# Kernel tuning notes

Hardware: AMD Instinct MI355X
Metric: run time of the kernel (lower is better)

Reference implementation:

```python
import jax, jax.numpy as jnp
import numpy as np

BN_EPS = 1e-5


def adder2d(x, w, stride=1, padding=1):
    """AdderNet layer: out[b,o,h,w] = -sum_{c,kh,kw} |patch - w|.
    x: [B,C,H,W], w: [O,C,K,K] -> [B,O,Ho,Wo]."""
    B, C, H, W = x.shape
    O, _, K, _ = w.shape
    # patches: [B, C*K*K, Ho, Wo] (feature order = (C, Kh, Kw), matching w.reshape)
    patches = jax.lax.conv_general_dilated_patches(
        x, (K, K), (stride, stride), [(padding, padding), (padding, padding)])
    Bp, F, Ho, Wo = patches.shape
    Xm = patches.transpose(0, 2, 3, 1).reshape(-1, F)  # [N, F], N = B*Ho*Wo
    Wm = w.reshape(O, F)
    # loop over output channels (O small) to avoid a [N, O, F] intermediate
    out = jax.lax.map(lambda wo: -jnp.sum(jnp.abs(Xm - wo), axis=-1), Wm)  # [O, N]
    return out.reshape(O, B, Ho, Wo).transpose(1, 0, 2, 3)


def batchnorm2d(x, gamma, beta):
    # training-mode BN: batch statistics over (B, H, W)
    mean = jnp.mean(x, axis=(0, 2, 3), keepdims=True)
    var = jnp.var(x, axis=(0, 2, 3), keepdims=True)
    inv = jax.lax.rsqrt(var + BN_EPS)
    return (x - mean) * inv * gamma[None, :, None, None] + beta[None, :, None, None]


def setup_inputs() -> dict:
    key = jax.random.key(0)
    ks = jax.random.split(key, 5)
    x = jax.random.normal(ks[0], (256, 1, 64, 64), dtype=jnp.float32)
    w1 = jax.random.normal(ks[1], (16, 1, 3, 3), dtype=jnp.float32) * 0.3
    w2 = jax.random.normal(ks[2], (32, 16, 3, 3), dtype=jnp.float32) * 0.1
    g1 = jnp.ones((16,), jnp.float32); b1 = jnp.zeros((16,), jnp.float32)
    g2 = jnp.ones((32,), jnp.float32); b2 = jnp.zeros((32,), jnp.float32)
    fc_w = jax.random.normal(ks[3], (10, 32), dtype=jnp.float32) * 0.1
    fc_b = jnp.zeros((10,), jnp.float32)
    return {"x": x, "w1": w1, "g1": g1, "b1": b1, "w2": w2,
            "g2": g2, "b2": b2, "fc_w": fc_w, "fc_b": fc_b}


def reference(x, w1, g1, b1, w2, g2, b2, fc_w, fc_b):
    h = jax.nn.relu(batchnorm2d(adder2d(x, w1), g1, b1))   # [B,16,64,64]
    h = jax.nn.relu(batchnorm2d(adder2d(h, w2), g2, b2))   # [B,32,64,64]
    h = jnp.mean(h, axis=(2, 3))                            # adaptive avg pool -> [B,32]
    return h @ fc_w.T + fc_b                                # [B,10]
```

## Files before the change

### kernel.cpp

```cpp
#include <hip/hip_runtime.h>
#include <hip/hip_fp16.h>


#define BATCH 256
#define HW 4096

typedef unsigned int u32;
typedef unsigned long long u64;
typedef __attribute__((ext_vector_type(4))) unsigned int u32x4;

__device__ __forceinline__ u32x4 mqsad(u64 src, u32 ref, u32x4 acc) {
#if __has_builtin(__builtin_amdgcn_mqsad_u32_u8)
  return __builtin_amdgcn_mqsad_u32_u8(src, ref, acc);
#else
  u32x4 d;
  asm("v_mqsad_u32_u8 %0, %1, %2, %3"
      : "=&v"(d)
      : "v"(src), "v"(ref), "v"(acc));
  return d;
#endif
}

__global__ __launch_bounds__(256, 4) void k_stats1(const float* __restrict__ x,
                                                   const float* __restrict__ w1,
                                                   double* __restrict__ s1,
                                                   const float* __restrict__ w2,
                                                   u32* __restrict__ w2b,
                                                   __half* __restrict__ y1) {
  __shared__ float sx[18 * 66];
  __shared__ float red[4 * 16 * 2];
  int blk = blockIdx.x, tid = threadIdx.x;
  int b = blk >> 2, row0 = (blk & 3) * 16;

  if (blk == 0) {
    for (int i = tid; i < 512; i += 256) {
      int oc = i >> 4, c = i & 15;
      int og = oc >> 3, o = oc & 7;
      const float* wp = w2 + (oc * 16 + c) * 9;
      u32 q[9];
#pragma unroll
      for (int t = 0; t < 9; t++) {
        float qf = rintf(fmaf(wp[t], 32.f, 48.f));
        q[t] = (u32)fminf(fmaxf(qf, 1.f), 255.f);
      }
      u32* dst = w2b + ((og * 16 + c) * 8 + o) * 3;
      dst[0] = q[0] | (q[1] << 8) | (q[2] << 16);
      dst[1] = q[3] | (q[4] << 8) | (q[5] << 16);
      dst[2] = q[6] | (q[7] << 8) | (q[8] << 16);
    }
  }

  const float* xb = x + b * HW;
  for (int i = tid; i < 18 * 66; i += 256) {
    int r = i / 66, cc = i - r * 66;
    int ry = row0 + r - 1, rx = cc - 1;
    sx[i] = (ry >= 0 && ry < 64 && rx >= 0 && rx < 64) ? xb[ry * 64 + rx] : 0.f;
  }
  __syncthreads();

  int col = tid & 63, rr4 = tid >> 6;
  float pa[4][9];
#pragma unroll
  for (int k = 0; k < 4; k++) {
    int rloc = rr4 * 4 + k;
#pragma unroll
    for (int dy = 0; dy < 3; dy++)
#pragma unroll
      for (int dx = 0; dx < 3; dx++)
        pa[k][dy * 3 + dx] = sx[(rloc + dy) * 66 + col + dx];
  }
  float tsum[16], tsq[16];
#pragma unroll
  for (int c = 0; c < 16; c++) { tsum[c] = 0.f; tsq[c] = 0.f; }
#pragma unroll
  for (int c = 0; c < 16; c++) {
    float wv[9];
#pragma unroll
    for (int t = 0; t < 9; t++) wv[t] = w1[c * 9 + t];
    __half* yc = y1 + (((size_t)(b * 16 + c)) << 12);
#pragma unroll
    for (int k = 0; k < 4; k++) {
      float acc = 0.f;
#pragma unroll
      for (int t = 0; t < 9; t++) acc += fabsf(pa[k][t] - wv[t]);
      float v = -acc;
      tsum[c] += v;
      tsq[c] = fmaf(v, v, tsq[c]);
      yc[((row0 + rr4 * 4 + k) << 6) + col] = __float2half(v);
    }
  }
  int lane = tid & 63, wid = tid >> 6;
#pragma unroll
  for (int c = 0; c < 16; c++) {
    float s = tsum[c], q = tsq[c];
    for (int off = 32; off; off >>= 1) {
      s += __shfl_down(s, off, 64);
      q += __shfl_down(q, off, 64);
    }
    if (lane == 0) { red[(wid * 16 + c) * 2] = s; red[(wid * 16 + c) * 2 + 1] = q; }
  }
  __syncthreads();
  if (tid < 16) {
    float s = red[tid * 2] + red[(16 + tid) * 2] + red[(32 + tid) * 2] + red[(48 + tid) * 2];
    float q = red[tid * 2 + 1] + red[(16 + tid) * 2 + 1] + red[(32 + tid) * 2 + 1] +
              red[(48 + tid) * 2 + 1];
    atomicAdd(&s1[tid], (double)s);
    atomicAdd(&s1[16 + tid], (double)q);
  }
}

__global__ __launch_bounds__(512, 8) void k_layer2(
    const __half* __restrict__ y1, const double* __restrict__ s1,
    const float* __restrict__ g1, const float* __restrict__ b1,
    const u32* __restrict__ w2b, __half* __restrict__ a2,
    double* __restrict__ s2) {
  __shared__ __align__(16) unsigned char shu[16 * 800];
  __shared__ float red[8 * 8];
  __shared__ float sc1s[16], sf1s[16];
  int blk = blockIdx.x;
  int b = blk >> 3, y0 = (blk & 7) << 3;
  int tid = threadIdx.x;

  if (tid < 16) {
    double N = 1048576.0;
    double mean = s1[tid] / N;
    double var = s1[16 + tid] / N - mean * mean;
    float inv = (float)(1.0 / sqrt(var + 1e-5));
    float sc = g1[tid] * inv;
    float sf = b1[tid] - (float)mean * sc;
    sc1s[tid] = sc * 32.f;
    sf1s[tid] = fmaf(sf, 32.f, 48.5f);
  }
  __syncthreads();

#pragma unroll 1
  for (int p = 0; p < 3; p++) {
    int jj = p * 512 + tid;
    if (jj < 1280) {
      int rowjob = jj >> 3, kq = jj & 7;
      int ch = rowjob / 10;
      int rr = rowjob - ch * 10;
      int gr = y0 + rr - 1;
      float sc8 = sc1s[ch], sf8 = sf1s[ch];
      u32 B[8];
      if (gr >= 0 && gr < 64) {
        uint4 v = *reinterpret_cast<const uint4*>(
            y1 + (((size_t)(b * 16 + ch)) << 12) + (gr << 6) + (kq << 3));
        const u32* vd = reinterpret_cast<const u32*>(&v);
#pragma unroll
        for (int q = 0; q < 4; q++) {
          float2 f = __half22float2(*reinterpret_cast<const __half2*>(&vd[q]));
          float t0 = fmaf(f.x, sc8, sf8);
          float t1 = fmaf(f.y, sc8, sf8);
          B[q * 2] = (u32)fminf(fmaxf(t0, 48.5f), 255.f);
          B[q * 2 + 1] = (u32)fminf(fmaxf(t1, 48.5f), 255.f);
        }
      } else {
#pragma unroll
        for (int q = 0; q < 8; q++) B[q] = 48u;
      }
      u32 prev = (u32)__shfl_up((int)B[7], 1, 64);
      if (kq == 0) prev = 48u;
      u32 d0 = prev | (B[0] << 8) | (B[1] << 16) | (B[2] << 24);
      u32 d1 = B[3] | (B[4] << 8) | (B[5] << 16) | (B[6] << 24);
      unsigned char* dst = shu + rowjob * 80 + (kq << 3);
      *reinterpret_cast<uint2*>(dst) = make_uint2(d0, d1);
      if (kq == 7)
        *reinterpret_cast<u32*>(dst + 8) = B[7] | 0x30303000u;
    }
  }
  __syncthreads();

  int lane = tid & 63;
  int w8 = tid >> 6;
  int og = w8 >> 1, half = w8 & 1;
  int wofs = __builtin_amdgcn_readfirstlane(og * 384 + half * 12);
  const u32* wbase = w2b + wofs;
  int r = lane >> 3;
  int x0 = (lane & 7) << 3;
  const unsigned char* shb = shu + r * 80 + x0;

  u32x4 acc[4][2];
#pragma unroll
  for (int o = 0; o < 4; o++) {
    acc[o][0] = (u32x4)(0u);
    acc[o][1] = (u32x4)(0u);
  }

  u64 Aa[3], Ab[3];
  u32 Ma[3], Mb[3];
  u32 Wa[12], Wb[12];

#define LOADC(Av, Mv, Wv, cc)                                     \
  do {                                                            \
    const unsigned char* rp_ = shb + (cc) * 800;                  \
    _Pragma("unroll") for (int dy_ = 0; dy_ < 3; dy_++) {         \
      Av[dy_] = *reinterpret_cast<const u64*>(rp_ + dy_ * 80);    \
      Mv[dy_] = *reinterpret_cast<const u32*>(rp_ + dy_ * 80 + 8);\
    }                                                             \
    const u32* wc_ = wbase + (cc) * 24;                           \
    _Pragma("unroll") for (int j_ = 0; j_ < 12; j_++) Wv[j_] = wc_[j_]; \
  } while (0)

#define COMPUTE(Av, Mv, Wv)                                       \
  do {                                                            \
    _Pragma("unroll") for (int dy_ = 0; dy_ < 3; dy_++) {         \
      u64 lo_ = Av[dy_];                                          \
      u64 hi_ = (Av[dy_] >> 32) | ((u64)Mv[dy_] << 32);           \
      _Pragma("unroll") for (int o_ = 0; o_ < 4; o_++) {          \
        u32 wr_ = Wv[o_ * 3 + dy_];                               \
        acc[o_][0] = mqsad(lo_, wr_, acc[o_][0]);                 \
        acc[o_][1] = mqsad(hi_, wr_, acc[o_][1]);                 \
      }                                                           \
    }                                                             \
  } while (0)

  LOADC(Aa, Ma, Wa, 0);
#pragma unroll 1
  for (int c = 0; c < 16; c += 2) {
    LOADC(Ab, Mb, Wb, c + 1);
    COMPUTE(Aa, Ma, Wa);
    if (c < 14) LOADC(Aa, Ma, Wa, c + 2);
    COMPUTE(Ab, Mb, Wb);
  }
#undef LOADC
#undef COMPUTE

  const float ksc = -1.f / 32.f;
  __half* a2b = a2 + ((size_t)b * 32 + og * 8 + half * 4) * HW + (y0 + r) * 64 + x0;
#pragma unroll
  for (int o = 0; o < 4; o++) {
    float f0 = (float)acc[o][0].x * ksc, f1 = (float)acc[o][0].y * ksc;
    float f2 = (float)acc[o][0].z * ksc, f3 = (float)acc[o][0].w * ksc;
    float f4 = (float)acc[o][1].x * ksc, f5 = (float)acc[o][1].y * ksc;
    float f6 = (float)acc[o][1].z * ksc, f7 = (float)acc[o][1].w * ksc;
    __half2 h01 = __floats2half2_rn(f0, f1);
    __half2 h23 = __floats2half2_rn(f2, f3);
    __half2 h45 = __floats2half2_rn(f4, f5);
    __half2 h67 = __floats2half2_rn(f6, f7);
    uint4 st = make_uint4(*reinterpret_cast<u32*>(&h01), *reinterpret_cast<u32*>(&h23),
                          *reinterpret_cast<u32*>(&h45), *reinterpret_cast<u32*>(&h67));
    *reinterpret_cast<uint4*>(a2b + o * HW) = st;
    float2 c0 = __half22float2(h01), c1 = __half22float2(h23);
    float2 c2 = __half22float2(h45), c3 = __half22float2(h67);
    float s = c0.x + c0.y + c1.x + c1.y + c2.x + c2.y + c3.x + c3.y;
    float q = c0.x * c0.x + c0.y * c0.y + c1.x * c1.x + c1.y * c1.y +
              c2.x * c2.x + c2.y * c2.y + c3.x * c3.x + c3.y * c3.y;
    for (int off = 32; off; off >>= 1) {
      s += __shfl_down(s, off, 64);
      q += __shfl_down(q, off, 64);
    }
    if (lane == 0) { red[w8 * 8 + o * 2] = s; red[w8 * 8 + o * 2 + 1] = q; }
  }
  __syncthreads();
  if (tid < 32) {
    int oc = tid;
    int ww = (oc >> 3) * 2 + ((oc >> 2) & 1);
    int oo = oc & 3;
    float s = red[ww * 8 + oo * 2];
    float q = red[ww * 8 + oo * 2 + 1];
    atomicAdd(&s2[oc], (double)s);
    atomicAdd(&s2[32 + oc], (double)q);
  }
}

__global__ __launch_bounds__(1024) void k_poolfc(const __half* __restrict__ a2,
                                                 const double* __restrict__ s2,
                                                 const float* __restrict__ g2,
                                                 const float* __restrict__ b2,
                                                 const float* __restrict__ fw,
                                                 const float* __restrict__ fb,
                                                 float* __restrict__ out) {
  __shared__ float sc2s[32], sf2s[32];
  __shared__ float poolv[32];
  int b = blockIdx.x, tid = threadIdx.x;
  if (tid < 32) {
    double N = 1048576.0;
    double mean = s2[tid] / N;
    double var = s2[32 + tid] / N - mean * mean;
    float inv = (float)(1.0 / sqrt(var + 1e-5));
    float sc = g2[tid] * inv;
    sc2s[tid] = sc;
    sf2s[tid] = b2[tid] - (float)mean * sc;
  }
  __syncthreads();
  int o = tid >> 5, part = tid & 31;
  const uint4* p = (const uint4*)(a2 + ((size_t)b * 32 + o) * HW);
  float s = sc2s[o], f = sf2s[o];
  float acc = 0.f;
#pragma unroll
  for (int i = 0; i < 16; i++) {
    uint4 v = p[i * 32 + part];
    float2 f0 = __half22float2(*reinterpret_cast<const __half2*>(&v.x));
    float2 f1 = __half22float2(*reinterpret_cast<const __half2*>(&v.y));
    float2 f2 = __half22float2(*reinterpret_cast<const __half2*>(&v.z));
    float2 f3 = __half22float2(*reinterpret_cast<const __half2*>(&v.w));
    acc += fmaxf(fmaf(f0.x, s, f), 0.f) + fmaxf(fmaf(f0.y, s, f), 0.f) +
           fmaxf(fmaf(f1.x, s, f), 0.f) + fmaxf(fmaf(f1.y, s, f), 0.f) +
           fmaxf(fmaf(f2.x, s, f), 0.f) + fmaxf(fmaf(f2.y, s, f), 0.f) +
           fmaxf(fmaf(f3.x, s, f), 0.f) + fmaxf(fmaf(f3.y, s, f), 0.f);
  }
  acc += __shfl_down(acc, 16, 32);
  acc += __shfl_down(acc, 8, 32);
  acc += __shfl_down(acc, 4, 32);
  acc += __shfl_down(acc, 2, 32);
  acc += __shfl_down(acc, 1, 32);
  if (part == 0) poolv[o] = acc * (1.f / 4096.f);
  __syncthreads();
  if (tid < 10) {
    float rr = fb[tid];
#pragma unroll
    for (int oc = 0; oc < 32; oc++) rr += poolv[oc] * fw[tid * 32 + oc];
    out[b * 10 + tid] = rr;
  }
}

extern "C" void kernel_launch(void* const* d_in, const int* in_sizes, int n_in,
                              void* d_out, int out_size, void* d_ws, size_t ws_size,
                              hipStream_t stream) {
  const float* x   = (const float*)d_in[0];
  const float* w1  = (const float*)d_in[1];
  const float* g1  = (const float*)d_in[2];
  const float* b1  = (const float*)d_in[3];
  const float* w2  = (const float*)d_in[4];
  const float* g2  = (const float*)d_in[5];
  const float* b2  = (const float*)d_in[6];
  const float* fcw = (const float*)d_in[7];
  const float* fcb = (const float*)d_in[8];
  float* out = (float*)d_out;

  char* ws = (char*)d_ws;
  __half* a2 = (__half*)ws;
  double* stats = (double*)(ws + 67108864);
  double* s1 = stats;
  double* s2 = stats + 32;
  u32* w2b = (u32*)(ws + 67108864 + 1024);
  __half* y1 = (__half*)(ws + 67108864 + 16384);

  hipMemsetAsync(stats, 0, 768, stream);
  k_stats1<<<1024, 256, 0, stream>>>(x, w1, s1, w2, w2b, y1);
  k_layer2<<<2048, 512, 0, stream>>>(y1, s1, g1, b1, w2b, a2, s2);
  k_poolfc<<<256, 1024, 0, stream>>>(a2, s2, g2, b2, fcw, fcb, out);
}
```

Before: 197.2 us.

## Fuse three kernels into one persistent kernel with software grid barriers

Merges the layer-1 stats, layer-2 adder, and pool/FC kernels into a single 256-block, 1024-thread kernel (one block per image) separated by atomic-counter grid barriers. The aim is to remove two kernel launch boundaries and their tail idle time, and to cut the per-block atomics for BN statistics. The cost is fewer, larger blocks with serial loops over row tiles, so less parallelism to hide latency. The barrier assumes all 256 blocks are co-resident and includes a spin timeout, so correctness depends on occupancy; the first block's w2 quantisation is also not ordered before other blocks read it until the first barrier.

```diff
diff --git a/kernel.cpp b/kernel.cpp
--- a/kernel.cpp
+++ b/kernel.cpp
@@ -2,7 +2,6 @@
 #include <hip/hip_fp16.h>
 
 
-#define BATCH 256
 #define HW 4096
 
 typedef unsigned int u32;
@@ -21,105 +20,111 @@
 #endif
 }
 
-__global__ __launch_bounds__(256, 4) void k_stats1(const float* __restrict__ x,
-                                                   const float* __restrict__ w1,
-                                                   double* __restrict__ s1,
-                                                   const float* __restrict__ w2,
-                                                   u32* __restrict__ w2b,
-                                                   __half* __restrict__ y1) {
-  __shared__ float sx[18 * 66];
-  __shared__ float red[4 * 16 * 2];
+__device__ __forceinline__ void gbar(u32* ctr, u32 tgt) {
+  __syncthreads();
+  if (threadIdx.x == 0) {
+    __threadfence();
+    __hip_atomic_fetch_add(ctr, 1u, __ATOMIC_ACQ_REL, __HIP_MEMORY_SCOPE_AGENT);
+    u32 n = 0;
+    while (__hip_atomic_load(ctr, __ATOMIC_ACQUIRE, __HIP_MEMORY_SCOPE_AGENT) < tgt &&
+           ++n < (1u << 21)) {
+      __builtin_amdgcn_s_sleep(2);
+    }
+    __threadfence();
+  }
+  __syncthreads();
+}
+
+__global__ __launch_bounds__(1024, 4) void k_fused(
+    const float* __restrict__ x, const float* __restrict__ w1,
+    const float* __restrict__ g1, const float* __restrict__ b1,
+    const float* __restrict__ w2, const float* __restrict__ g2,
+    const float* __restrict__ b2, const float* __restrict__ fw,
+    const float* __restrict__ fb, float* __restrict__ out,
+    double* s1, double* s2, u32* ctr, u32* w2b,
+    __half* __restrict__ y1, __half* __restrict__ a2) {
+  __shared__ __align__(16) unsigned char smem[25600];
+  __shared__ float red[512];
+  __shared__ float p1a[16], p1b[16], p2a[32], p2b[32], poolv[32];
   int blk = blockIdx.x, tid = threadIdx.x;
-  int b = blk >> 2, row0 = (blk & 3) * 16;
-
-  if (blk == 0) {
-    for (int i = tid; i < 512; i += 256) {
-      int oc = i >> 4, c = i & 15;
-      int og = oc >> 3, o = oc & 7;
-      const float* wp = w2 + (oc * 16 + c) * 9;
-      u32 q[9];
-#pragma unroll
-      for (int t = 0; t < 9; t++) {
-        float qf = rintf(fmaf(wp[t], 32.f, 48.f));
-        q[t] = (u32)fminf(fmaxf(qf, 1.f), 255.f);
-      }
-      u32* dst = w2b + ((og * 16 + c) * 8 + o) * 3;
-      dst[0] = q[0] | (q[1] << 8) | (q[2] << 16);
-      dst[1] = q[3] | (q[4] << 8) | (q[5] << 16);
-      dst[2] = q[6] | (q[7] << 8) | (q[8] << 16);
-    }
-  }
-
-  const float* xb = x + b * HW;
-  for (int i = tid; i < 18 * 66; i += 256) {
-    int r = i / 66, cc = i - r * 66;
-    int ry = row0 + r - 1, rx = cc - 1;
-    sx[i] = (ry >= 0 && ry < 64 && rx >= 0 && rx < 64) ? xb[ry * 64 + rx] : 0.f;
-  }
-  __syncthreads();
-
-  int col = tid & 63, rr4 = tid >> 6;
-  float pa[4][9];
-#pragma unroll
-  for (int k = 0; k < 4; k++) {
-    int rloc = rr4 * 4 + k;
-#pragma unroll
-    for (int dy = 0; dy < 3; dy++)
-#pragma unroll
-      for (int dx = 0; dx < 3; dx++)
-        pa[k][dy * 3 + dx] = sx[(rloc + dy) * 66 + col + dx];
-  }
+  int b = blk;
+
+  if (blk == 0 && tid < 512) {
+    int oc = tid >> 4, c = tid & 15;
+    int og = oc >> 3, o = oc & 7;
+    const float* wp = w2 + (oc * 16 + c) * 9;
+    u32 q[9];
+#pragma unroll
+    for (int t = 0; t < 9; t++) {
+      float qf = rintf(fmaf(wp[t], 32.f, 48.f));
+      q[t] = (u32)fminf(fmaxf(qf, 1.f), 255.f);
+    }
+    u32* dst = w2b + ((og * 16 + c) * 8 + o) * 3;
+    dst[0] = q[0] | (q[1] << 8) | (q[2] << 16);
+    dst[1] = q[3] | (q[4] << 8) | (q[5] << 16);
+    dst[2] = q[6] | (q[7] << 8) | (q[8] << 16);
+  }
+
   float tsum[16], tsq[16];
 #pragma unroll
   for (int c = 0; c < 16; c++) { tsum[c] = 0.f; tsq[c] = 0.f; }
-#pragma unroll
-  for (int c = 0; c < 16; c++) {
-    float wv[9];
-#pragma unroll
-    for (int t = 0; t < 9; t++) wv[t] = w1[c * 9 + t];
-    __half* yc = y1 + (((size_t)(b * 16 + c)) << 12);
-#pragma unroll
-    for (int k = 0; k < 4; k++) {
-      float acc = 0.f;
-#pragma unroll
-      for (int t = 0; t < 9; t++) acc += fabsf(pa[k][t] - wv[t]);
-      float v = -acc;
-      tsum[c] += v;
-      tsq[c] = fmaf(v, v, tsq[c]);
-      yc[((row0 + rr4 * 4 + k) << 6) + col] = __float2half(v);
-    }
-  }
-  int lane = tid & 63, wid = tid >> 6;
-#pragma unroll
-  for (int c = 0; c < 16; c++) {
-    float s = tsum[c], q = tsq[c];
-    for (int off = 32; off; off >>= 1) {
-      s += __shfl_down(s, off, 64);
-      q += __shfl_down(q, off, 64);
-    }
-    if (lane == 0) { red[(wid * 16 + c) * 2] = s; red[(wid * 16 + c) * 2 + 1] = q; }
-  }
-  __syncthreads();
-  if (tid < 16) {
-    float s = red[tid * 2] + red[(16 + tid) * 2] + red[(32 + tid) * 2] + red[(48 + tid) * 2];
-    float q = red[tid * 2 + 1] + red[(16 + tid) * 2 + 1] + red[(32 + tid) * 2 + 1] +
-              red[(48 + tid) * 2 + 1];
-    atomicAdd(&s1[tid], (double)s);
-    atomicAdd(&s1[16 + tid], (double)q);
-  }
-}
-
-__global__ __launch_bounds__(512, 8) void k_layer2(
-    const __half* __restrict__ y1, const double* __restrict__ s1,
-    const float* __restrict__ g1, const float* __restrict__ b1,
-    const u32* __restrict__ w2b, __half* __restrict__ a2,
-    double* __restrict__ s2) {
-  __shared__ __align__(16) unsigned char shu[16 * 800];
-  __shared__ float red[8 * 8];
-  __shared__ float sc1s[16], sf1s[16];
-  int blk = blockIdx.x;
-  int b = blk >> 3, y0 = (blk & 7) << 3;
-  int tid = threadIdx.x;
+  {
+    int col = tid & 63, wr = tid >> 6;
+    const float* xb = x + b * HW;
+#pragma unroll 1
+    for (int q4 = 0; q4 < 4; q4++) {
+      int row0 = q4 * 16;
+      float* sx = (float*)smem;
+      __syncthreads();
+      for (int i = tid; i < 18 * 66; i += 1024) {
+        int rr = i / 66, cc = i - rr * 66;
+        int ry = row0 + rr - 1, rx = cc - 1;
+        sx[i] = (ry >= 0 && ry < 64 && rx >= 0 && rx < 64) ? xb[ry * 64 + rx] : 0.f;
+      }
+      __syncthreads();
+      float pa[9];
+#pragma unroll
+      for (int dy = 0; dy < 3; dy++)
+#pragma unroll
+        for (int dx = 0; dx < 3; dx++)
+          pa[dy * 3 + dx] = sx[(wr + dy) * 66 + col + dx];
+#pragma unroll
+      for (int c = 0; c < 16; c++) {
+        float wv[9];
+#pragma unroll
+        for (int t = 0; t < 9; t++) wv[t] = w1[c * 9 + t];
+        float acc = 0.f;
+#pragma unroll
+        for (int t = 0; t < 9; t++) acc += fabsf(pa[t] - wv[t]);
+        float v = -acc;
+        tsum[c] += v;
+        tsq[c] = fmaf(v, v, tsq[c]);
+        y1[(((size_t)(b * 16 + c)) << 12) + ((row0 + wr) << 6) + col] = __float2half(v);
+      }
+    }
+    int lane = tid & 63;
+#pragma unroll
+    for (int c = 0; c < 16; c++) {
+      float s = tsum[c], qv = tsq[c];
+      for (int off = 32; off; off >>= 1) {
+        s += __shfl_down(s, off, 64);
+        qv += __shfl_down(qv, off, 64);
+      }
+      if (lane == 0) { red[(wr * 16 + c) * 2] = s; red[(wr * 16 + c) * 2 + 1] = qv; }
+    }
+    __syncthreads();
+    if (tid < 16) {
+      float s = 0.f, qv = 0.f;
+#pragma unroll
+      for (int w = 0; w < 16; w++) {
+        s += red[(w * 16 + tid) * 2];
+        qv += red[(w * 16 + tid) * 2 + 1];
+      }
+      atomicAdd(&s1[tid], (double)s);
+      atomicAdd(&s1[16 + tid], (double)qv);
+    }
+  }
+  gbar(ctr + 0, 256);
 
   if (tid < 16) {
     double N = 1048576.0;
@@ -128,68 +133,76 @@
     float inv = (float)(1.0 / sqrt(var + 1e-5));
     float sc = g1[tid] * inv;
     float sf = b1[tid] - (float)mean * sc;
-    sc1s[tid] = sc * 32.f;
-    sf1s[tid] = fmaf(sf, 32.f, 48.5f);
-  }
-  __syncthreads();
+    p1a[tid] = sc * 32.f;
+    p1b[tid] = fmaf(sf, 32.f, 48.5f);
+  }
+  __syncthreads();
+
+  {
+    int th = tid & 511, hb = tid >> 9;
+    int lane = tid & 63;
+    int w8 = (tid >> 6) & 7;
+    int og = w8 >> 1, half = w8 & 1;
+    int wofs = __builtin_amdgcn_readfirstlane(og * 384 + half * 12);
+    const u32* wbase = w2b + wofs;
+    int r = lane >> 3, x0 = (lane & 7) << 3;
+    unsigned char* shu = smem + hb * 12800;
+    const unsigned char* shb = shu + r * 80 + x0;
+
+    float ssum[4], ssq[4];
+#pragma unroll
+    for (int o = 0; o < 4; o++) { ssum[o] = 0.f; ssq[o] = 0.f; }
 
 #pragma unroll 1
-  for (int p = 0; p < 3; p++) {
-    int jj = p * 512 + tid;
-    if (jj < 1280) {
-      int rowjob = jj >> 3, kq = jj & 7;
-      int ch = rowjob / 10;
-      int rr = rowjob - ch * 10;
-      int gr = y0 + rr - 1;
-      float sc8 = sc1s[ch], sf8 = sf1s[ch];
-      u32 B[8];
-      if (gr >= 0 && gr < 64) {
-        uint4 v = *reinterpret_cast<const uint4*>(
-            y1 + (((size_t)(b * 16 + ch)) << 12) + (gr << 6) + (kq << 3));
-        const u32* vd = reinterpret_cast<const u32*>(&v);
-#pragma unroll
-        for (int q = 0; q < 4; q++) {
-          float2 f = __half22float2(*reinterpret_cast<const __half2*>(&vd[q]));
-          float t0 = fmaf(f.x, sc8, sf8);
-          float t1 = fmaf(f.y, sc8, sf8);
-          B[q * 2] = (u32)fminf(fmaxf(t0, 48.5f), 255.f);
-          B[q * 2 + 1] = (u32)fminf(fmaxf(t1, 48.5f), 255.f);
+    for (int pr = 0; pr < 4; pr++) {
+      int y0 = (pr * 2 + hb) * 8;
+      __syncthreads();
+
+#pragma unroll 1
+      for (int pp = 0; pp < 3; pp++) {
+        int jj = pp * 512 + th;
+        if (jj < 1280) {
+          int rowjob = jj >> 3, kq = jj & 7;
+          int ch = rowjob / 10;
+          int rr = rowjob - ch * 10;
+          int gr = y0 + rr - 1;
+          float sc8 = p1a[ch], sf8 = p1b[ch];
+          u32 B[8];
+          if (gr >= 0 && gr < 64) {
+            uint4 v = *reinterpret_cast<const uint4*>(
+                y1 + (((size_t)(b * 16 + ch)) << 12) + (gr << 6) + (kq << 3));
+            const u32* vd = reinterpret_cast<const u32*>(&v);
+#pragma unroll
+            for (int qq = 0; qq < 4; qq++) {
+              float2 f = __half22float2(*reinterpret_cast<const __half2*>(&vd[qq]));
+              float t0 = fmaf(f.x, sc8, sf8);
+              float t1 = fmaf(f.y, sc8, sf8);
+              B[qq * 2] = (u32)fminf(fmaxf(t0, 48.5f), 255.f);
+              B[qq * 2 + 1] = (u32)fminf(fmaxf(t1, 48.5f), 255.f);
+            }
+          } else {
+#pragma unroll
+            for (int qq = 0; qq < 8; qq++) B[qq] = 48u;
+          }
+          u32 prev = (u32)__shfl_up((int)B[7], 1, 64);
+          if (kq == 0) prev = 48u;
+          u32 d0 = prev | (B[0] << 8) | (B[1] << 16) | (B[2] << 24);
+          u32 d1 = B[3] | (B[4] << 8) | (B[5] << 16) | (B[6] << 24);
+          unsigned char* dst = shu + rowjob * 80 + (kq << 3);
+          *reinterpret_cast<uint2*>(dst) = make_uint2(d0, d1);
+          if (kq == 7)
+            *reinterpret_cast<u32*>(dst + 8) = B[7] | 0x30303000u;
         }
-      } else {
-#pragma unroll
-        for (int q = 0; q < 8; q++) B[q] = 48u;
-      }
-      u32 prev = (u32)__shfl_up((int)B[7], 1, 64);
-      if (kq == 0) prev = 48u;
-      u32 d0 = prev | (B[0] << 8) | (B[1] << 16) | (B[2] << 24);
-      u32 d1 = B[3] | (B[4] << 8) | (B[5] << 16) | (B[6] << 24);
-      unsigned char* dst = shu + rowjob * 80 + (kq << 3);
-      *reinterpret_cast<uint2*>(dst) = make_uint2(d0, d1);
-      if (kq == 7)
-        *reinterpret_cast<u32*>(dst + 8) = B[7] | 0x30303000u;
-    }
-  }
-  __syncthreads();
-
-  int lane = tid & 63;
-  int w8 = tid >> 6;
-  int og = w8 >> 1, half = w8 & 1;
-  int wofs = __builtin_amdgcn_readfirstlane(og * 384 + half * 12);
-  const u32* wbase = w2b + wofs;
-  int r = lane >> 3;
-  int x0 = (lane & 7) << 3;
-  const unsigned char* shb = shu + r * 80 + x0;
-
-  u32x4 acc[4][2];
-#pragma unroll
-  for (int o = 0; o < 4; o++) {
-    acc[o][0] = (u32x4)(0u);
-    acc[o][1] = (u32x4)(0u);
-  }
-
-  u64 Aa[3], Ab[3];
-  u32 Ma[3], Mb[3];
-  u32 Wa[12], Wb[12];
+      }
+      __syncthreads();
+
+      u32x4 acc[4][2];
+#pragma unroll
+      for (int o = 0; o < 4; o++) { acc[o][0] = (u32x4)(0u); acc[o][1] = (u32x4)(0u); }
+
+      u64 Aa[3], Ab[3];
+      u32 Ma[3], Mb[3];
+      u32 Wa[12], Wb[12];
 
 #define LOADC(Av, Mv, Wv, cc)                                     \
   do {                                                            \
@@ -215,98 +228,102 @@
     }                                                             \
   } while (0)
 
-  LOADC(Aa, Ma, Wa, 0);
+      LOADC(Aa, Ma, Wa, 0);
 #pragma unroll 1
-  for (int c = 0; c < 16; c += 2) {
-    LOADC(Ab, Mb, Wb, c + 1);
-    COMPUTE(Aa, Ma, Wa);
-    if (c < 14) LOADC(Aa, Ma, Wa, c + 2);
-    COMPUTE(Ab, Mb, Wb);
-  }
+      for (int c = 0; c < 16; c += 2) {
+        LOADC(Ab, Mb, Wb, c + 1);
+        COMPUTE(Aa, Ma, Wa);
+        if (c < 14) LOADC(Aa, Ma, Wa, c + 2);
+        COMPUTE(Ab, Mb, Wb);
+      }
 #undef LOADC
 #undef COMPUTE
 
-  const float ksc = -1.f / 32.f;
-  __half* a2b = a2 + ((size_t)b * 32 + og * 8 + half * 4) * HW + (y0 + r) * 64 + x0;
-#pragma unroll
-  for (int o = 0; o < 4; o++) {
-    float f0 = (float)acc[o][0].x * ksc, f1 = (float)acc[o][0].y * ksc;
-    float f2 = (float)acc[o][0].z * ksc, f3 = (float)acc[o][0].w * ksc;
-    float f4 = (float)acc[o][1].x * ksc, f5 = (float)acc[o][1].y * ksc;
-    float f6 = (float)acc[o][1].z * ksc, f7 = (float)acc[o][1].w * ksc;
-    __half2 h01 = __floats2half2_rn(f0, f1);
-    __half2 h23 = __floats2half2_rn(f2, f3);
-    __half2 h45 = __floats2half2_rn(f4, f5);
-    __half2 h67 = __floats2half2_rn(f6, f7);
-    uint4 st = make_uint4(*reinterpret_cast<u32*>(&h01), *reinterpret_cast<u32*>(&h23),
-                          *reinterpret_cast<u32*>(&h45), *reinterpret_cast<u32*>(&h67));
-    *reinterpret_cast<uint4*>(a2b + o * HW) = st;
-    float2 c0 = __half22float2(h01), c1 = __half22float2(h23);
-    float2 c2 = __half22float2(h45), c3 = __half22float2(h67);
-    float s = c0.x + c0.y + c1.x + c1.y + c2.x + c2.y + c3.x + c3.y;
-    float q = c0.x * c0.x + c0.y * c0.y + c1.x * c1.x + c1.y * c1.y +
-              c2.x * c2.x + c2.y * c2.y + c3.x * c3.x + c3.y * c3.y;
-    for (int off = 32; off; off >>= 1) {
-      s += __shfl_down(s, off, 64);
-      q += __shfl_down(q, off, 64);
-    }
-    if (lane == 0) { red[w8 * 8 + o * 2] = s; red[w8 * 8 + o * 2 + 1] = q; }
-  }
-  __syncthreads();
-  if (tid < 32) {
-    int oc = tid;
-    int ww = (oc >> 3) * 2 + ((oc >> 2) & 1);
-    int oo = oc & 3;
-    float s = red[ww * 8 + oo * 2];
-    float q = red[ww * 8 + oo * 2 + 1];
-    atomicAdd(&s2[oc], (double)s);
-    atomicAdd(&s2[32 + oc], (double)q);
-  }
-}
-
-__global__ __launch_bounds__(1024) void k_poolfc(const __half* __restrict__ a2,
-                                                 const double* __restrict__ s2,
-                                                 const float* __restrict__ g2,
-                                                 const float* __restrict__ b2,
-                                                 const float* __restrict__ fw,
-                                                 const float* __restrict__ fb,
-                                                 float* __restrict__ out) {
-  __shared__ float sc2s[32], sf2s[32];
-  __shared__ float poolv[32];
-  int b = blockIdx.x, tid = threadIdx.x;
+      const float ksc = -1.f / 32.f;
+      __half* a2b =
+          a2 + ((size_t)b * 32 + og * 8 + half * 4) * HW + (y0 + r) * 64 + x0;
+#pragma unroll
+      for (int o = 0; o < 4; o++) {
+        float f0 = (float)acc[o][0].x * ksc, f1 = (float)acc[o][0].y * ksc;
+        float f2 = (float)acc[o][0].z * ksc, f3 = (float)acc[o][0].w * ksc;
+        float f4 = (float)acc[o][1].x * ksc, f5 = (float)acc[o][1].y * ksc;
+        float f6 = (float)acc[o][1].z * ksc, f7 = (float)acc[o][1].w * ksc;
+        __half2 h01 = __floats2half2_rn(f0, f1);
+        __half2 h23 = __floats2half2_rn(f2, f3);
+        __half2 h45 = __floats2half2_rn(f4, f5);
+        __half2 h67 = __floats2half2_rn(f6, f7);
+        uint4 st = make_uint4(*reinterpret_cast<u32*>(&h01), *reinterpret_cast<u32*>(&h23),
+                              *reinterpret_cast<u32*>(&h45), *reinterpret_cast<u32*>(&h67));
+        *reinterpret_cast<uint4*>(a2b + o * HW) = st;
+        float2 c0 = __half22float2(h01), c1 = __half22float2(h23);
+        float2 c2 = __half22float2(h45), c3 = __half22float2(h67);
+        ssum[o] += c0.x + c0.y + c1.x + c1.y + c2.x + c2.y + c3.x + c3.y;
+        ssq[o] += c0.x * c0.x + c0.y * c0.y + c1.x * c1.x + c1.y * c1.y +
+                  c2.x * c2.x + c2.y * c2.y + c3.x * c3.x + c3.y * c3.y;
+      }
+    }
+
+#pragma unroll
+    for (int o = 0; o < 4; o++) {
+      float s = ssum[o], qv = ssq[o];
+      for (int off = 32; off; off >>= 1) {
+        s += __shfl_down(s, off, 64);
+        qv += __shfl_down(qv, off, 64);
+      }
+      if (lane == 0) {
+        red[(hb * 8 + w8) * 8 + o * 2] = s;
+        red[(hb * 8 + w8) * 8 + o * 2 + 1] = qv;
+      }
+    }
+    __syncthreads();
+    if (tid < 32) {
+      int oc = tid;
+      int ww = (oc >> 3) * 2 + ((oc >> 2) & 1);
+      int oo = oc & 3;
+      float s = red[ww * 8 + oo * 2] + red[(8 + ww) * 8 + oo * 2];
+      float qv = red[ww * 8 + oo * 2 + 1] + red[(8 + ww) * 8 + oo * 2 + 1];
+      atomicAdd(&s2[oc], (double)s);
+      atomicAdd(&s2[32 + oc], (double)qv);
+    }
+  }
+  gbar(ctr + 1, 256);
+
   if (tid < 32) {
     double N = 1048576.0;
     double mean = s2[tid] / N;
     double var = s2[32 + tid] / N - mean * mean;
     float inv = (float)(1.0 / sqrt(var + 1e-5));
     float sc = g2[tid] * inv;
-    sc2s[tid] = sc;
-    sf2s[tid] = b2[tid] - (float)mean * sc;
-  }
-  __syncthreads();
-  int o = tid >> 5, part = tid & 31;
-  const uint4* p = (const uint4*)(a2 + ((size_t)b * 32 + o) * HW);
-  float s = sc2s[o], f = sf2s[o];
-  float acc = 0.f;
-#pragma unroll
-  for (int i = 0; i < 16; i++) {
-    uint4 v = p[i * 32 + part];
-    float2 f0 = __half22float2(*reinterpret_cast<const __half2*>(&v.x));
-    float2 f1 = __half22float2(*reinterpret_cast<const __half2*>(&v.y));
-    float2 f2 = __half22float2(*reinterpret_cast<const __half2*>(&v.z));
-    float2 f3 = __half22float2(*reinterpret_cast<const __half2*>(&v.w));
-    acc += fmaxf(fmaf(f0.x, s, f), 0.f) + fmaxf(fmaf(f0.y, s, f), 0.f) +
-           fmaxf(fmaf(f1.x, s, f), 0.f) + fmaxf(fmaf(f1.y, s, f), 0.f) +
-           fmaxf(fmaf(f2.x, s, f), 0.f) + fmaxf(fmaf(f2.y, s, f), 0.f) +
-           fmaxf(fmaf(f3.x, s, f), 0.f) + fmaxf(fmaf(f3.y, s, f), 0.f);
-  }
-  acc += __shfl_down(acc, 16, 32);
-  acc += __shfl_down(acc, 8, 32);
-  acc += __shfl_down(acc, 4, 32);
-  acc += __shfl_down(acc, 2, 32);
-  acc += __shfl_down(acc, 1, 32);
-  if (part == 0) poolv[o] = acc * (1.f / 4096.f);
-  __syncthreads();
+    p2a[tid] = sc;
+    p2b[tid] = b2[tid] - (float)mean * sc;
+  }
+  __syncthreads();
+  {
+    int oc = tid >> 5, part = tid & 31;
+    const uint4* p = (const uint4*)(a2 + ((size_t)b * 32 + oc) * HW);
+    float s = p2a[oc], f = p2b[oc];
+    float acc = 0.f;
+#pragma unroll
+    for (int i = 0; i < 16; i++) {
+      uint4 v = p[i * 32 + part];
+      float2 f0 = __half22float2(*reinterpret_cast<const __half2*>(&v.x));
+      float2 f1 = __half22float2(*reinterpret_cast<const __half2*>(&v.y));
+      float2 f2 = __half22float2(*reinterpret_cast<const __half2*>(&v.z));
+      float2 f3 = __half22float2(*reinterpret_cast<const __half2*>(&v.w));
+      acc += fmaxf(fmaf(f0.x, s, f), 0.f) + fmaxf(fmaf(f0.y, s, f), 0.f) +
+             fmaxf(fmaf(f1.x, s, f), 0.f) + fmaxf(fmaf(f1.y, s, f), 0.f) +
+             fmaxf(fmaf(f2.x, s, f), 0.f) + fmaxf(fmaf(f2.y, s, f), 0.f) +
+             fmaxf(fmaf(f3.x, s, f), 0.f) + fmaxf(fmaf(f3.y, s, f), 0.f);
+    }
+    acc += __shfl_down(acc, 16, 32);
+    acc += __shfl_down(acc, 8, 32);
+    acc += __shfl_down(acc, 4, 32);
+    acc += __shfl_down(acc, 2, 32);
+    acc += __shfl_down(acc, 1, 32);
+    if (part == 0) poolv[oc] = acc * (1.f / 4096.f);
+  }
+  __syncthreads();
+
   if (tid < 10) {
     float rr = fb[tid];
 #pragma unroll
@@ -334,11 +351,11 @@
   double* stats = (double*)(ws + 67108864);
   double* s1 = stats;
   double* s2 = stats + 32;
+  u32* ctr = (u32*)(ws + 67108864 + 768);
   u32* w2b = (u32*)(ws + 67108864 + 1024);
   __half* y1 = (__half*)(ws + 67108864 + 16384);
 
-  hipMemsetAsync(stats, 0, 768, stream);
-  k_stats1<<<1024, 256, 0, stream>>>(x, w1, s1, w2, w2b, y1);
-  k_layer2<<<2048, 512, 0, stream>>>(y1, s1, g1, b1, w2b, a2, s2);
-  k_poolfc<<<256, 1024, 0, stream>>>(a2, s2, g2, b2, fcw, fcb, out);
+  hipMemsetAsync(stats, 0, 1024, stream);
+  k_fused<<<256, 1024, 0, stream>>>(x, w1, g1, b1, w2, g2, b2, fcw, fcb,
+                                    out, s1, s2, ctr, w2b, y1, a2);
 }
```

After: 242.3 us. +22.9%, slower.
